# Performance work log

Measured on AMD Instinct MI355X. Metric: run time of the kernel, lower is better.

## Reference

```python
import jax, jax.numpy as jnp
import numpy as np

N_USER = 27094
M_SPOT = 42852
N_EDGE = 2_000_000
D_FEAT = 128


def setup_inputs() -> dict:
    key = jax.random.key(0)
    k1, k2, k3, k4 = jax.random.split(key, 4)
    spot_x = jax.random.normal(k1, (M_SPOT, D_FEAT), dtype=jnp.float32)
    user_x = jax.random.normal(k2, (N_USER, D_FEAT), dtype=jnp.float32)
    u_idx = jax.random.randint(k3, (N_EDGE,), 0, N_USER, dtype=jnp.int32)
    s_idx = jax.random.randint(k4, (N_EDGE,), 0, M_SPOT, dtype=jnp.int32)
    user_spot = jnp.stack([u_idx, s_idx], axis=0)  # [2, E]
    return {"spot_x": spot_x, "user_x": user_x, "user_spot": user_spot}


def reference(spot_x, user_x, user_spot):
    u = user_spot[0]  # [E] user index per edge
    s = user_spot[1]  # [E] spot index per edge
    # symmetric GCN normalization: 1/sqrt(deg_u * deg_s) per edge
    user_deg = jnp.bincount(u, length=N_USER)
    spot_deg = jnp.bincount(s, length=M_SPOT)
    div = jnp.sqrt((user_deg[u] * spot_deg[s]).astype(spot_x.dtype))[:, None]  # [E,1]
    # spot -> user aggregation
    source_spot = spot_x[s] / div                                   # [E, D]
    user_out = jax.ops.segment_sum(source_spot, u, num_segments=N_USER)
    # user -> spot aggregation
    source_user = user_x[u] / div                                   # [E, D]
    spot_out = jax.ops.segment_sum(source_user, s, num_segments=M_SPOT)
    return (spot_out, user_out)
```

## Files before the change

### kernel.cpp

```cpp
#include <hip/hip_runtime.h>
#include <stdint.h>


#define NPB_LOG2 6
#define NPB 64
#define MAXB 768
#define PART_CHUNK 2048
#define BH_CHUNK 16384
#define SORT_CAP 8192
#define SORT2_CAP 16384

__device__ __forceinline__ ushort f2bf(float f) {
    uint32_t u = __float_as_uint(f);
    return (ushort)((u + 0x7fffu + ((u >> 16) & 1u)) >> 16);
}

__global__ __launch_bounds__(256) void bhist_kernel(
        const int* __restrict__ u, const int* __restrict__ s, int E,
        int nbu, int nbs, int* __restrict__ bd) {
    __shared__ int hist[2 * MAXB];
    const int tid = threadIdx.x;
    const int nb = nbu + nbs;
    const int beg = blockIdx.x * BH_CHUNK;
    const int end = min(beg + BH_CHUNK, E);
    for (int b = tid; b < nb; b += 256) hist[b] = 0;
    __syncthreads();
    for (int i = beg + tid; i < end; i += 256) {
        atomicAdd(&hist[u[i] >> NPB_LOG2], 1);
        atomicAdd(&hist[nbu + (s[i] >> NPB_LOG2)], 1);
    }
    __syncthreads();
    for (int b = tid; b < nb; b += 256) {
        int h = hist[b];
        if (h) atomicAdd(&bd[b], h);
    }
}

__global__ __launch_bounds__(1024) void scan2_kernel(
        const int* __restrict__ bd, int nbu, int nbs,
        int* __restrict__ buoff, int* __restrict__ bsoff,
        int* __restrict__ gcu, int* __restrict__ gcs) {
    __shared__ int wsums[16];
    __shared__ int total;
    const int tid = threadIdx.x, lane = tid & 63, wid = tid >> 6;
    const int n   = blockIdx.x ? nbs : nbu;
    const int* in = blockIdx.x ? (bd + nbu) : bd;
    int* out = blockIdx.x ? bsoff : buoff;
    int* gc  = blockIdx.x ? gcs   : gcu;
    int v = (tid < n) ? in[tid] : 0;
    int x = v;
#pragma unroll
    for (int d = 1; d < 64; d <<= 1) {
        int t = __shfl_up(x, d);
        if (lane >= d) x += t;
    }
    if (lane == 63) wsums[wid] = x;
    __syncthreads();
    if (tid == 0) {
        int run = 0;
#pragma unroll
        for (int w = 0; w < 16; ++w) { int t = wsums[w]; wsums[w] = run; run += t; }
        total = run;
    }
    __syncthreads();
    int excl = wsums[wid] + (x - v);
    if (tid < n) { out[tid] = excl; gc[tid] = excl; }
    if (tid == 0) out[n] = total;
}

__global__ void convert_kernel(const float* __restrict__ x, const float* __restrict__ isd,
                               ushort* __restrict__ xb, int n_rows) {
    int idx = blockIdx.x * blockDim.x + threadIdx.x;
    if (idx >= (n_rows << 6)) return;
    int row = idx >> 6, c = idx & 63;
    float w = isd[row];
    const float* xr = x + ((size_t)row << 7);
    ushort2 o;
    o.x = f2bf(xr[c] * w);
    o.y = f2bf(xr[c + 64] * w);
    *reinterpret_cast<ushort2*>(xb + ((size_t)row << 7) + 2 * c) = o;
}

__global__ __launch_bounds__(256) void part_kernel(
        const int* __restrict__ prim, const int* __restrict__ sec, int E,
        int nb, int* __restrict__ gcur, uint32_t* __restrict__ out) {
    __shared__ int hist[MAXB];
    __shared__ int loff[MAXB];
    __shared__ int gbase[MAXB];
    __shared__ int cur[MAXB];
    __shared__ int wsum[4];
    __shared__ uint32_t sbuf[PART_CHUNK];
    const int tid = threadIdx.x;
    const int lane = tid & 63;
    const int wid = tid >> 6;
    const int beg = blockIdx.x * PART_CHUNK;
    const int end = min(beg + PART_CHUNK, E);
    const int cnt_total = end - beg;
    for (int b = tid; b < nb; b += 256) hist[b] = 0;
    __syncthreads();
    for (int i = beg + tid; i < end; i += 256)
        atomicAdd(&hist[prim[i] >> NPB_LOG2], 1);
    __syncthreads();
    {
        int b0 = tid * 3;
        int h0 = (b0 + 0 < nb) ? hist[b0 + 0] : 0;
        int h1 = (b0 + 1 < nb) ? hist[b0 + 1] : 0;
        int h2 = (b0 + 2 < nb) ? hist[b0 + 2] : 0;
        int tsum = h0 + h1 + h2;
        int x = tsum;
#pragma unroll
        for (int d = 1; d < 64; d <<= 1) {
            int t = __shfl_up(x, d);
            if (lane >= d) x += t;
        }
        if (lane == 63) wsum[wid] = x;
        __syncthreads();
        if (tid == 0) {
            int run = 0;
#pragma unroll
            for (int w = 0; w < 4; ++w) { int t = wsum[w]; wsum[w] = run; run += t; }
        }
        __syncthreads();
        int base = wsum[wid] + (x - tsum);
        if (b0 + 0 < nb) loff[b0 + 0] = base;
        if (b0 + 1 < nb) loff[b0 + 1] = base + h0;
        if (b0 + 2 < nb) loff[b0 + 2] = base + h0 + h1;
    }
    __syncthreads();
    for (int b = tid; b < nb; b += 256) {
        cur[b] = loff[b];
        int c = hist[b];
        gbase[b] = c > 0 ? atomicAdd(&gcur[b], c) : 0;
    }
    __syncthreads();
    for (int i = beg + tid; i < end; i += 256) {
        int p = prim[i], s = sec[i];
        int b = p >> NPB_LOG2;
        int l = atomicAdd(&cur[b], 1);
        sbuf[l] = ((uint32_t)p << 16) | (uint32_t)s;
    }
    __syncthreads();
    for (int k = tid; k < cnt_total; k += 256) {
        uint32_t p = sbuf[k];
        int b = (int)(p >> (16 + NPB_LOG2));
        out[gbase[b] + (k - loff[b])] = p;
    }
}

__global__ __launch_bounds__(256) void bdeg2_kernel(
        const uint32_t* __restrict__ bufU, const uint32_t* __restrict__ bufS,
        const int* __restrict__ buoff, const int* __restrict__ bsoff, int nbu,
        float* __restrict__ isd_u, float* __restrict__ isd_s, int N, int M) {
    __shared__ int hist[NPB];
    const int tid = threadIdx.x;
    const int b = blockIdx.x;
    const uint32_t* buf; const int* boff; float* isd; int n_rows; int bb;
    if (b < nbu) { buf = bufU; boff = buoff; isd = isd_u; n_rows = N; bb = b; }
    else         { buf = bufS; boff = bsoff; isd = isd_s; n_rows = M; bb = b - nbu; }
    const int jbeg = boff[bb];
    const int cnt = boff[bb + 1] - jbeg;
    if (tid < NPB) hist[tid] = 0;
    __syncthreads();
    for (int k = tid; k < cnt; k += 256)
        atomicAdd(&hist[(buf[jbeg + k] >> 16) & (NPB - 1)], 1);
    __syncthreads();
    if (tid < NPB) {
        int node = (bb << NPB_LOG2) + tid;
        if (node < n_rows) {
            int h = hist[tid];
            isd[node] = h > 0 ? rsqrtf((float)h) : 0.f;
        }
    }
}

__global__ __launch_bounds__(512) void fscan2_kernel(
        const ushort* __restrict__ xbs, const ushort* __restrict__ xbu,
        const uint32_t* __restrict__ bufU, const uint32_t* __restrict__ bufS,
        const int* __restrict__ buoff, const int* __restrict__ bsoff, int nbu,
        float* __restrict__ user_out, float* __restrict__ spot_out) {
    __shared__ ushort srt[SORT2_CAP];
    __shared__ int hist[NPB];
    __shared__ int scur[NPB];
    __shared__ float isdl[NPB];
    const int tid = threadIdx.x;
    const int b = blockIdx.x;
    const ushort* xb; const uint32_t* buf; const int* boff; float* out; int bb;
    if (b < nbu) { xb = xbs; buf = bufU; boff = buoff; out = user_out; bb = b; }
    else         { xb = xbu; buf = bufS; boff = bsoff; out = spot_out; bb = b - nbu; }
    const int jbeg = boff[bb];
    const int cnt = boff[bb + 1] - jbeg;
    if (cnt <= 0) return;
    const bool fits = (cnt <= SORT2_CAP);
    if (tid < NPB) hist[tid] = 0;
    __syncthreads();
    for (int k = tid; k < cnt; k += 512)
        atomicAdd(&hist[(buf[jbeg + k] >> 16) & (NPB - 1)], 1);
    __syncthreads();
    if (tid < NPB) {
        int h = hist[tid];
        int x = h;
#pragma unroll
        for (int d = 1; d < 64; d <<= 1) {
            int t = __shfl_up(x, d);
            if (tid >= d) x += t;
        }
        scur[tid] = x - h;
        isdl[tid] = h > 0 ? rsqrtf((float)h) : 0.f;
    }
    __syncthreads();
    if (fits) {
        for (int k = tid; k < cnt; k += 512) {
            uint32_t p = buf[jbeg + k];
            int slot = atomicAdd(&scur[(p >> 16) & (NPB - 1)], 1);
            srt[slot] = (ushort)p;
        }
    }
    __syncthreads();
    const int wid = tid >> 6, lane = tid & 63;
    const int rowbase = bb << NPB_LOG2;

#define ROWX(sv) (*reinterpret_cast<const uint32_t*>( \
        xb + (((size_t)(sv)) << 7) + (lane << 1)))
#define UPX(rv) __uint_as_float((rv) << 16)
#define UPY(rv) __uint_as_float((rv) & 0xffff0000u)

    if (fits) {
        for (int ld = wid; ld < NPB; ld += 8) {
            const int deg = hist[ld];
            if (!deg) continue;
            const int off0 = scur[ld] - deg;
            const float w = isdl[ld];
            float ax = 0.f, ay = 0.f;
            int j = 0;
            if (deg >= 16) {
                ushort c0 = srt[off0+0], c1 = srt[off0+1], c2 = srt[off0+2], c3 = srt[off0+3],
                       c4 = srt[off0+4], c5 = srt[off0+5], c6 = srt[off0+6], c7 = srt[off0+7];
                uint32_t r0 = ROWX(c0), r1 = ROWX(c1), r2 = ROWX(c2), r3 = ROWX(c3),
                         r4 = ROWX(c4), r5 = ROWX(c5), r6 = ROWX(c6), r7 = ROWX(c7);
                for (j = 8; j + 8 <= deg; j += 8) {
                    const int q = off0 + j;
                    ushort n0 = srt[q+0], n1 = srt[q+1], n2 = srt[q+2], n3 = srt[q+3],
                           n4 = srt[q+4], n5 = srt[q+5], n6 = srt[q+6], n7 = srt[q+7];
                    uint32_t s0 = ROWX(n0), s1 = ROWX(n1), s2 = ROWX(n2), s3 = ROWX(n3),
                             s4 = ROWX(n4), s5 = ROWX(n5), s6 = ROWX(n6), s7 = ROWX(n7);
                    ax += ((UPX(r0) + UPX(r1)) + (UPX(r2) + UPX(r3)))
                        + ((UPX(r4) + UPX(r5)) + (UPX(r6) + UPX(r7)));
                    ay += ((UPY(r0) + UPY(r1)) + (UPY(r2) + UPY(r3)))
                        + ((UPY(r4) + UPY(r5)) + (UPY(r6) + UPY(r7)));
                    r0 = s0; r1 = s1; r2 = s2; r3 = s3;
                    r4 = s4; r5 = s5; r6 = s6; r7 = s7;
                }
                ax += ((UPX(r0) + UPX(r1)) + (UPX(r2) + UPX(r3)))
                    + ((UPX(r4) + UPX(r5)) + (UPX(r6) + UPX(r7)));
                ay += ((UPY(r0) + UPY(r1)) + (UPY(r2) + UPY(r3)))
                    + ((UPY(r4) + UPY(r5)) + (UPY(r6) + UPY(r7)));
            }
            for (; j < deg; ++j) {
                uint32_t r = ROWX(srt[off0 + j]);
                ax += UPX(r); ay += UPY(r);
            }
            const size_t ro = ((size_t)(rowbase + ld)) << 7;
            out[ro + lane]      = ax * w;
            out[ro + 64 + lane] = ay * w;
        }
    } else {
        const int cs = (cnt + 7) >> 3;
        const int beg = wid * cs;
        const int end = min(beg + cs, cnt);
        if (beg >= end) return;
        float ax = 0.f, ay = 0.f;
        int curd = (int)(buf[jbeg + beg] >> 16);
        for (int k = beg; k < end; ++k) {
            uint32_t p = buf[jbeg + k];
            int d_ = (int)(p >> 16);
            if (d_ != curd) {
                float w_ = isdl[curd & (NPB - 1)];
                unsafeAtomicAdd(out + ((size_t)curd << 7) + lane, ax * w_);
                unsafeAtomicAdd(out + ((size_t)curd << 7) + 64 + lane, ay * w_);
                ax = 0.f; ay = 0.f; curd = d_;
            }
            uint32_t r = ROWX((ushort)p);
            ax += UPX(r); ay += UPY(r);
        }
        float w_ = isdl[curd & (NPB - 1)];
        unsafeAtomicAdd(out + ((size_t)curd << 7) + lane, ax * w_);
        unsafeAtomicAdd(out + ((size_t)curd << 7) + 64 + lane, ay * w_);
    }
#undef UPY
#undef UPX
#undef ROWX
}


__global__ __launch_bounds__(256) void bdeg_kernel(
        const uint32_t* __restrict__ buf, const int* __restrict__ boff,
        float* __restrict__ isd, int n_rows) {
    __shared__ int hist[NPB];
    const int tid = threadIdx.x;
    const int jbeg = boff[blockIdx.x];
    const int cnt = boff[blockIdx.x + 1] - jbeg;
    if (tid < NPB) hist[tid] = 0;
    __syncthreads();
    for (int k = tid; k < cnt; k += 256)
        atomicAdd(&hist[(buf[jbeg + k] >> 16) & (NPB - 1)], 1);
    __syncthreads();
    if (tid < NPB) {
        int node = (blockIdx.x << NPB_LOG2) + tid;
        if (node < n_rows) {
            int h = hist[tid];
            isd[node] = h > 0 ? rsqrtf((float)h) : 0.f;
        }
    }
}

__global__ __launch_bounds__(512) void fscan_kernel(
        const ushort* __restrict__ xb, const uint32_t* __restrict__ buf,
        const int* __restrict__ boff, float* __restrict__ isd_out,
        float* __restrict__ out, int n_rows) {
    __shared__ uint32_t sorted[SORT_CAP];
    __shared__ int hist[NPB];
    __shared__ int scur[NPB];
    __shared__ float isdl[NPB];
    const int tid = threadIdx.x;
    const int jbeg = boff[blockIdx.x];
    const int cnt = boff[blockIdx.x + 1] - jbeg;
    if (cnt <= 0) {
        if (tid < NPB) {
            int node = (blockIdx.x << NPB_LOG2) + tid;
            if (node < n_rows) isd_out[node] = 0.f;
        }
        return;
    }
    const bool fits = (cnt <= SORT_CAP);
    if (tid < NPB) hist[tid] = 0;
    __syncthreads();
    for (int k = tid; k < cnt; k += 512)
        atomicAdd(&hist[(buf[jbeg + k] >> 16) & (NPB - 1)], 1);
    __syncthreads();
    if (tid < NPB) {
        int h = hist[tid];
        int x = h;
#pragma unroll
        for (int d = 1; d < 64; d <<= 1) {
            int t = __shfl_up(x, d);
            if (tid >= d) x += t;
        }
        scur[tid] = x - h;
        float iv = h > 0 ? rsqrtf((float)h) : 0.f;
        isdl[tid] = iv;
        int node = (blockIdx.x << NPB_LOG2) + tid;
        if (node < n_rows) isd_out[node] = iv;
    }
    __syncthreads();
    if (fits) {
        for (int k = tid; k < cnt; k += 512) {
            uint32_t p = buf[jbeg + k];
            int slot = atomicAdd(&scur[(p >> 16) & (NPB - 1)], 1);
            sorted[slot] = p;
        }
    }
    __syncthreads();
    const int wid = tid >> 6, lane = tid & 63;
    const int cs = (cnt + 7) >> 3;
    const int beg = wid * cs;
    const int end = min(beg + cs, cnt);
    if (beg >= end) return;

#define QLD(i) (fits ? sorted[i] : buf[jbeg + (i)])
#define ROW(pv) (*reinterpret_cast<const uint32_t*>( \
        xb + (((size_t)((pv) & 0xffffu)) << 7) + (lane << 1)))
#define UPX(rv) __uint_as_float((rv) << 16)
#define UPY(rv) __uint_as_float((rv) & 0xffff0000u)
    float ax = 0.f, ay = 0.f;
    int curd = (int)(QLD(beg) >> 16);
    for (int k = beg; k < end; ++k) {
        uint32_t p = QLD(k);
        int d_ = (int)(p >> 16);
        if (d_ != curd) {
            float w_ = isdl[curd & (NPB - 1)];
            unsafeAtomicAdd(out + ((size_t)curd << 7) + lane, ax * w_);
            unsafeAtomicAdd(out + ((size_t)curd << 7) + 64 + lane, ay * w_);
            ax = 0.f; ay = 0.f; curd = d_;
        }
        uint32_t r = ROW(p);
        ax += UPX(r); ay += UPY(r);
    }
    float w_ = isdl[curd & (NPB - 1)];
    unsafeAtomicAdd(out + ((size_t)curd << 7) + lane, ax * w_);
    unsafeAtomicAdd(out + ((size_t)curd << 7) + 64 + lane, ay * w_);
#undef UPY
#undef UPX
#undef ROW
#undef QLD
}


__global__ void deg_kernel(const int* __restrict__ u, const int* __restrict__ s,
                           int E, int* __restrict__ udeg, int* __restrict__ sdeg) {
    int i = blockIdx.x * blockDim.x + threadIdx.x;
    if (i < E) {
        atomicAdd(&udeg[u[i]], 1);
        atomicAdd(&sdeg[s[i]], 1);
    }
}

__global__ void init_isd_kernel(const int* __restrict__ udeg, const int* __restrict__ sdeg,
                                float* __restrict__ isd_u, float* __restrict__ isd_s,
                                int n_user, int m_spot) {
    int i = blockIdx.x * blockDim.x + threadIdx.x;
    if (i < n_user) { int d = udeg[i]; isd_u[i] = d > 0 ? rsqrtf((float)d) : 0.f; }
    if (i < m_spot) { int d = sdeg[i]; isd_s[i] = d > 0 ? rsqrtf((float)d) : 0.f; }
}

__global__ __launch_bounds__(256) void scatter_kernel(const float* __restrict__ spot_x,
                                                      const float* __restrict__ user_x,
                                                      const int* __restrict__ u,
                                                      const int* __restrict__ s, int E,
                                                      const float* __restrict__ isd_u,
                                                      const float* __restrict__ isd_s,
                                                      float* __restrict__ spot_out,
                                                      float* __restrict__ user_out) {
    const int lane = threadIdx.x & 63;
    const int e = blockIdx.x * 4 + (threadIdx.x >> 6);
    if (e >= E) return;
    const int uu = u[e], ss = s[e];
    const float w = isd_u[uu] * isd_s[ss];
    const float2 sv = *reinterpret_cast<const float2*>(spot_x + (size_t)ss * 128 + lane * 2);
    const float2 uv = *reinterpret_cast<const float2*>(user_x + (size_t)uu * 128 + lane * 2);
    atomicAdd(&user_out[(size_t)uu * 128 + lane * 2 + 0], sv.x * w);
    atomicAdd(&user_out[(size_t)uu * 128 + lane * 2 + 1], sv.y * w);
    atomicAdd(&spot_out[(size_t)ss * 128 + lane * 2 + 0], uv.x * w);
    atomicAdd(&spot_out[(size_t)ss * 128 + lane * 2 + 1], uv.y * w);
}

static inline char* align256(char* p) {
    return (char*)(((uintptr_t)p + 255u) & ~(uintptr_t)255u);
}

extern "C" void kernel_launch(void* const* d_in, const int* in_sizes, int n_in,
                              void* d_out, int out_size, void* d_ws, size_t ws_size,
                              hipStream_t stream) {
    const float* spot_x = (const float*)d_in[0];
    const float* user_x = (const float*)d_in[1];
    const int*   edges  = (const int*)d_in[2];
    const int M = in_sizes[0] / 128;
    const int N = in_sizes[1] / 128;
    const int E = in_sizes[2] / 2;
    const int* u = edges;
    const int* s = edges + E;
    float* spot_out = (float*)d_out;
    float* user_out = (float*)d_out + (size_t)M * 128;

    const int nbu = (N + NPB - 1) / NPB;
    const int nbs = (M + NPB - 1) / NPB;
    const int nm = (N > M) ? N : M;
    const int gpart = (E + PART_CHUNK - 1) / PART_CHUNK;

    char* ws = (char*)d_ws;
    float*    isd_u = (float*)ws; ws = align256(ws + sizeof(float) * (size_t)N);
    float*    isd_s = (float*)ws; ws = align256(ws + sizeof(float) * (size_t)M);
    int*      bd    = (int*)ws;   ws = align256(ws + sizeof(int) * (size_t)(nbu + nbs));
    int*      buoff = (int*)ws;   ws = align256(ws + sizeof(int) * (size_t)(nbu + 1));
    int*      bsoff = (int*)ws;   ws = align256(ws + sizeof(int) * (size_t)(nbs + 1));
    int*      gcu   = (int*)ws;   ws = align256(ws + sizeof(int) * (size_t)nbu);
    int*      gcs   = (int*)ws;   ws = align256(ws + sizeof(int) * (size_t)nbs);
    uint32_t* bufU  = (uint32_t*)ws; ws = align256(ws + sizeof(uint32_t) * (size_t)E);
    uint32_t* bufS  = (uint32_t*)ws; ws = align256(ws + sizeof(uint32_t) * (size_t)E);
    ushort*   xbs   = (ushort*)ws;
    ushort*   xbu   = (ushort*)align256((char*)xbs + sizeof(ushort) * ((size_t)M * 128));
    size_t tierA_needed = (size_t)((char*)xbu - (char*)d_ws)
                        + sizeof(ushort) * ((size_t)N * 128);
    size_t tierB_needed = (size_t)((char*)xbs - (char*)d_ws)
                        + sizeof(ushort) * ((size_t)nm * 128);

    if (tierB_needed <= ws_size && nbu <= MAXB && nbs <= MAXB) {
        hipMemsetAsync(bd, 0, sizeof(int) * (size_t)(nbu + nbs), stream);
        hipMemsetAsync(d_out, 0, sizeof(float) * (size_t)out_size, stream);
        bhist_kernel<<<(E + BH_CHUNK - 1) / BH_CHUNK, 256, 0, stream>>>(
            u, s, E, nbu, nbs, bd);
        scan2_kernel<<<2, 1024, 0, stream>>>(bd, nbu, nbs, buoff, bsoff, gcu, gcs);
        part_kernel<<<gpart, 256, 0, stream>>>(u, s, E, nbu, gcu, bufU);
        part_kernel<<<gpart, 256, 0, stream>>>(s, u, E, nbs, gcs, bufS);
        if (tierA_needed <= ws_size) {
            bdeg2_kernel<<<nbu + nbs, 256, 0, stream>>>(
                bufU, bufS, buoff, bsoff, nbu, isd_u, isd_s, N, M);
            convert_kernel<<<((M << 6) + 255) / 256, 256, 0, stream>>>(spot_x, isd_s, xbs, M);
            convert_kernel<<<((N << 6) + 255) / 256, 256, 0, stream>>>(user_x, isd_u, xbu, N);
            fscan2_kernel<<<nbu + nbs, 512, 0, stream>>>(
                xbs, xbu, bufU, bufS, buoff, bsoff, nbu, user_out, spot_out);
        } else {
            ushort* xb = xbs;
            bdeg_kernel<<<nbs, 256, 0, stream>>>(bufS, bsoff, isd_s, M);
            convert_kernel<<<((M << 6) + 255) / 256, 256, 0, stream>>>(spot_x, isd_s, xb, M);
            fscan_kernel<<<nbu, 512, 0, stream>>>(xb, bufU, buoff, isd_u, user_out, N);
            convert_kernel<<<((N << 6) + 255) / 256, 256, 0, stream>>>(user_x, isd_u, xb, N);
            fscan_kernel<<<nbs, 512, 0, stream>>>(xb, bufS, bsoff, isd_s, spot_out, M);
        }
        return;
    }

    {
        char* w2 = (char*)d_ws;
        int*   udeg2  = (int*)w2;   w2 += sizeof(int) * (size_t)N;
        int*   sdeg2  = (int*)w2;   w2 += sizeof(int) * (size_t)M;
        float* isd_u2 = (float*)w2; w2 += sizeof(float) * (size_t)N;
        float* isd_s2 = (float*)w2; w2 += sizeof(float) * (size_t)M;
        if ((size_t)(w2 - (char*)d_ws) <= ws_size) {
            hipMemsetAsync(udeg2, 0, sizeof(int) * (size_t)(N + M), stream);
            deg_kernel<<<(E + 255) / 256, 256, 0, stream>>>(u, s, E, udeg2, sdeg2);
            init_isd_kernel<<<(nm + 255) / 256, 256, 0, stream>>>(
                udeg2, sdeg2, isd_u2, isd_s2, N, M);
            hipMemsetAsync(d_out, 0, sizeof(float) * (size_t)out_size, stream);
            scatter_kernel<<<((size_t)E + 3) / 4, 256, 0, stream>>>(
                spot_x, user_x, u, s, E, isd_u2, isd_s2, spot_out, user_out);
        }
    }
}
```

Before: 282.0 us.

## Split gather buckets across multiple blocks, merge partition and convert kernels

The per-bucket gather kernel is replaced by one that splits each 64-node bucket across several blocks (about 2048 blocks per direction). Each block register-sorts its slice and accumulates into the output with atomic adds instead of plain stores. The two partition launches are fused into one kernel that reads u and s once, and the two convert launches are merged into one. The goals are more parallelism and occupancy in the gather phase and fewer launches and index reads. In exchange, the gather now issues more global float atomics on rows shared between sub-blocks and uses more shared memory in the partition kernel.

```diff
diff --git a/kernel.cpp b/kernel.cpp
--- a/kernel.cpp
+++ b/kernel.cpp
@@ -8,7 +8,7 @@
 #define PART_CHUNK 2048
 #define BH_CHUNK 16384
 #define SORT_CAP 8192
-#define SORT2_CAP 16384
+#define RCAP 4096
 
 __device__ __forceinline__ ushort f2bf(float f) {
     uint32_t u = __float_as_uint(f);
@@ -68,6 +68,24 @@
     if (tid == 0) out[n] = total;
 }
 
+__global__ void convert2_kernel(const float* __restrict__ spot_x,
+                                const float* __restrict__ user_x,
+                                const float* __restrict__ isd_s,
+                                const float* __restrict__ isd_u,
+                                ushort* __restrict__ xbs, ushort* __restrict__ xbu,
+                                int M, int N) {
+    int idx = blockIdx.x * blockDim.x + threadIdx.x;
+    if (idx >= ((M + N) << 6)) return;
+    int row = idx >> 6, c = idx & 63;
+    const float* x; float w; ushort* xb;
+    if (row < M) { x = spot_x + ((size_t)row << 7); w = isd_s[row]; xb = xbs + ((size_t)row << 7); }
+    else { row -= M; x = user_x + ((size_t)row << 7); w = isd_u[row]; xb = xbu + ((size_t)row << 7); }
+    ushort2 o;
+    o.x = f2bf(x[c] * w);
+    o.y = f2bf(x[c + 64] * w);
+    *reinterpret_cast<ushort2*>(xb + 2 * c) = o;
+}
+
 __global__ void convert_kernel(const float* __restrict__ x, const float* __restrict__ isd,
                                ushort* __restrict__ xb, int n_rows) {
     int idx = blockIdx.x * blockDim.x + threadIdx.x;
@@ -81,27 +99,33 @@
     *reinterpret_cast<ushort2*>(xb + ((size_t)row << 7) + 2 * c) = o;
 }
 
-__global__ __launch_bounds__(256) void part_kernel(
-        const int* __restrict__ prim, const int* __restrict__ sec, int E,
-        int nb, int* __restrict__ gcur, uint32_t* __restrict__ out) {
-    __shared__ int hist[MAXB];
-    __shared__ int loff[MAXB];
-    __shared__ int gbase[MAXB];
-    __shared__ int cur[MAXB];
+__global__ __launch_bounds__(256) void part2_kernel(
+        const int* __restrict__ u, const int* __restrict__ s, int E,
+        int nbu, int nbs, int* __restrict__ gcu, int* __restrict__ gcs,
+        uint32_t* __restrict__ outU, uint32_t* __restrict__ outS) {
+    __shared__ int histU[MAXB], loffU[MAXB], gbaseU[MAXB], curU[MAXB];
+    __shared__ int histS[MAXB], loffS[MAXB], gbaseS[MAXB], curS[MAXB];
     __shared__ int wsum[4];
-    __shared__ uint32_t sbuf[PART_CHUNK];
+    __shared__ uint32_t sbufU[PART_CHUNK];
+    __shared__ uint32_t sbufS[PART_CHUNK];
     const int tid = threadIdx.x;
     const int lane = tid & 63;
     const int wid = tid >> 6;
     const int beg = blockIdx.x * PART_CHUNK;
     const int end = min(beg + PART_CHUNK, E);
     const int cnt_total = end - beg;
-    for (int b = tid; b < nb; b += 256) hist[b] = 0;
-    __syncthreads();
-    for (int i = beg + tid; i < end; i += 256)
-        atomicAdd(&hist[prim[i] >> NPB_LOG2], 1);
-    __syncthreads();
-    {
+    for (int b = tid; b < nbu; b += 256) histU[b] = 0;
+    for (int b = tid; b < nbs; b += 256) histS[b] = 0;
+    __syncthreads();
+    for (int i = beg + tid; i < end; i += 256) {
+        atomicAdd(&histU[u[i] >> NPB_LOG2], 1);
+        atomicAdd(&histS[s[i] >> NPB_LOG2], 1);
+    }
+    __syncthreads();
+    for (int dir = 0; dir < 2; ++dir) {
+        int nb = dir ? nbs : nbu;
+        int* hist = dir ? histS : histU;
+        int* loff = dir ? loffS : loffU;
         int b0 = tid * 3;
         int h0 = (b0 + 0 < nb) ? hist[b0 + 0] : 0;
         int h1 = (b0 + 1 < nb) ? hist[b0 + 1] : 0;
@@ -125,25 +149,34 @@
         if (b0 + 0 < nb) loff[b0 + 0] = base;
         if (b0 + 1 < nb) loff[b0 + 1] = base + h0;
         if (b0 + 2 < nb) loff[b0 + 2] = base + h0 + h1;
-    }
-    __syncthreads();
-    for (int b = tid; b < nb; b += 256) {
-        cur[b] = loff[b];
-        int c = hist[b];
-        gbase[b] = c > 0 ? atomicAdd(&gcur[b], c) : 0;
+        __syncthreads();
+    }
+    for (int b = tid; b < nbu; b += 256) {
+        curU[b] = loffU[b];
+        int c = histU[b];
+        gbaseU[b] = c > 0 ? atomicAdd(&gcu[b], c) : 0;
+    }
+    for (int b = tid; b < nbs; b += 256) {
+        curS[b] = loffS[b];
+        int c = histS[b];
+        gbaseS[b] = c > 0 ? atomicAdd(&gcs[b], c) : 0;
     }
     __syncthreads();
     for (int i = beg + tid; i < end; i += 256) {
-        int p = prim[i], s = sec[i];
-        int b = p >> NPB_LOG2;
-        int l = atomicAdd(&cur[b], 1);
-        sbuf[l] = ((uint32_t)p << 16) | (uint32_t)s;
+        int uu = u[i], ss = s[i];
+        int lu = atomicAdd(&curU[uu >> NPB_LOG2], 1);
+        sbufU[lu] = ((uint32_t)uu << 16) | (uint32_t)ss;
+        int ls = atomicAdd(&curS[ss >> NPB_LOG2], 1);
+        sbufS[ls] = ((uint32_t)ss << 16) | (uint32_t)uu;
     }
     __syncthreads();
     for (int k = tid; k < cnt_total; k += 256) {
-        uint32_t p = sbuf[k];
+        uint32_t p = sbufU[k];
         int b = (int)(p >> (16 + NPB_LOG2));
-        out[gbase[b] + (k - loff[b])] = p;
+        outU[gbaseU[b] + (k - loffU[b])] = p;
+        uint32_t q = sbufS[k];
+        int b2 = (int)(q >> (16 + NPB_LOG2));
+        outS[gbaseS[b2] + (k - loffS[b2])] = q;
     }
 }
 
@@ -173,63 +206,69 @@
     }
 }
 
-__global__ __launch_bounds__(512) void fscan2_kernel(
-        const ushort* __restrict__ xbs, const ushort* __restrict__ xbu,
-        const uint32_t* __restrict__ bufU, const uint32_t* __restrict__ bufS,
-        const int* __restrict__ buoff, const int* __restrict__ bsoff, int nbu,
-        float* __restrict__ user_out, float* __restrict__ spot_out) {
-    __shared__ ushort srt[SORT2_CAP];
+__global__ __launch_bounds__(512) void fscan3_kernel(
+        const ushort* __restrict__ xb, const uint32_t* __restrict__ buf,
+        const int* __restrict__ boff, const float* __restrict__ isd,
+        float* __restrict__ out, int split) {
+    __shared__ ushort srt[RCAP];
     __shared__ int hist[NPB];
     __shared__ int scur[NPB];
-    __shared__ float isdl[NPB];
     const int tid = threadIdx.x;
-    const int b = blockIdx.x;
-    const ushort* xb; const uint32_t* buf; const int* boff; float* out; int bb;
-    if (b < nbu) { xb = xbs; buf = bufU; boff = buoff; out = user_out; bb = b; }
-    else         { xb = xbu; buf = bufS; boff = bsoff; out = spot_out; bb = b - nbu; }
-    const int jbeg = boff[bb];
-    const int cnt = boff[bb + 1] - jbeg;
+    const int bucket = blockIdx.x / split;
+    const int sub = blockIdx.x - bucket * split;
+    const int jb = boff[bucket];
+    const int cnt = boff[bucket + 1] - jb;
     if (cnt <= 0) return;
-    const bool fits = (cnt <= SORT2_CAP);
-    if (tid < NPB) hist[tid] = 0;
-    __syncthreads();
-    for (int k = tid; k < cnt; k += 512)
-        atomicAdd(&hist[(buf[jbeg + k] >> 16) & (NPB - 1)], 1);
-    __syncthreads();
-    if (tid < NPB) {
-        int h = hist[tid];
-        int x = h;
-#pragma unroll
-        for (int d = 1; d < 64; d <<= 1) {
-            int t = __shfl_up(x, d);
-            if (tid >= d) x += t;
-        }
-        scur[tid] = x - h;
-        isdl[tid] = h > 0 ? rsqrtf((float)h) : 0.f;
-    }
-    __syncthreads();
-    if (fits) {
-        for (int k = tid; k < cnt; k += 512) {
-            uint32_t p = buf[jbeg + k];
-            int slot = atomicAdd(&scur[(p >> 16) & (NPB - 1)], 1);
-            srt[slot] = (ushort)p;
-        }
-    }
-    __syncthreads();
+    const int sbeg = jb + (int)((long long)cnt * sub / split);
+    const int send = jb + (int)((long long)cnt * (sub + 1) / split);
+    const int scnt = send - sbeg;
+    if (scnt <= 0) return;
     const int wid = tid >> 6, lane = tid & 63;
-    const int rowbase = bb << NPB_LOG2;
+    const int rowbase = bucket << NPB_LOG2;
 
 #define ROWX(sv) (*reinterpret_cast<const uint32_t*>( \
         xb + (((size_t)(sv)) << 7) + (lane << 1)))
 #define UPX(rv) __uint_as_float((rv) << 16)
 #define UPY(rv) __uint_as_float((rv) & 0xffff0000u)
 
-    if (fits) {
+    if (scnt <= RCAP) {
+        if (tid < NPB) hist[tid] = 0;
+        __syncthreads();
+        uint32_t ereg[8];
+#pragma unroll
+        for (int k = 0; k < 8; ++k) {
+            int idx = sbeg + (k << 9) + tid;
+            if (idx < send) {
+                ereg[k] = buf[idx];
+                atomicAdd(&hist[(ereg[k] >> 16) & (NPB - 1)], 1);
+            } else ereg[k] = 0u;
+        }
+        __syncthreads();
+        if (tid < NPB) {
+            int h = hist[tid];
+            int x = h;
+#pragma unroll
+            for (int d = 1; d < 64; d <<= 1) {
+                int t = __shfl_up(x, d);
+                if (tid >= d) x += t;
+            }
+            scur[tid] = x - h;
+        }
+        __syncthreads();
+#pragma unroll
+        for (int k = 0; k < 8; ++k) {
+            int idx = sbeg + (k << 9) + tid;
+            if (idx < send) {
+                uint32_t p = ereg[k];
+                int slot = atomicAdd(&scur[(p >> 16) & (NPB - 1)], 1);
+                srt[slot] = (ushort)p;
+            }
+        }
+        __syncthreads();
         for (int ld = wid; ld < NPB; ld += 8) {
             const int deg = hist[ld];
             if (!deg) continue;
             const int off0 = scur[ld] - deg;
-            const float w = isdl[ld];
             float ax = 0.f, ay = 0.f;
             int j = 0;
             if (deg >= 16) {
@@ -259,22 +298,23 @@
                 uint32_t r = ROWX(srt[off0 + j]);
                 ax += UPX(r); ay += UPY(r);
             }
+            const float w = isd[rowbase + ld];
             const size_t ro = ((size_t)(rowbase + ld)) << 7;
-            out[ro + lane]      = ax * w;
-            out[ro + 64 + lane] = ay * w;
+            unsafeAtomicAdd(out + ro + lane,      ax * w);
+            unsafeAtomicAdd(out + ro + 64 + lane, ay * w);
         }
     } else {
-        const int cs = (cnt + 7) >> 3;
-        const int beg = wid * cs;
-        const int end = min(beg + cs, cnt);
+        const int cs = (scnt + 7) >> 3;
+        const int beg = sbeg + wid * cs;
+        const int end = min(beg + cs, send);
         if (beg >= end) return;
         float ax = 0.f, ay = 0.f;
-        int curd = (int)(buf[jbeg + beg] >> 16);
+        int curd = (int)(buf[beg] >> 16);
         for (int k = beg; k < end; ++k) {
-            uint32_t p = buf[jbeg + k];
+            uint32_t p = buf[k];
             int d_ = (int)(p >> 16);
             if (d_ != curd) {
-                float w_ = isdl[curd & (NPB - 1)];
+                float w_ = isd[curd];
                 unsafeAtomicAdd(out + ((size_t)curd << 7) + lane, ax * w_);
                 unsafeAtomicAdd(out + ((size_t)curd << 7) + 64 + lane, ay * w_);
                 ax = 0.f; ay = 0.f; curd = d_;
@@ -282,7 +322,7 @@
             uint32_t r = ROWX((ushort)p);
             ax += UPX(r); ay += UPY(r);
         }
-        float w_ = isdl[curd & (NPB - 1)];
+        float w_ = isd[curd];
         unsafeAtomicAdd(out + ((size_t)curd << 7) + lane, ax * w_);
         unsafeAtomicAdd(out + ((size_t)curd << 7) + 64 + lane, ay * w_);
     }
@@ -479,15 +519,18 @@
         bhist_kernel<<<(E + BH_CHUNK - 1) / BH_CHUNK, 256, 0, stream>>>(
             u, s, E, nbu, nbs, bd);
         scan2_kernel<<<2, 1024, 0, stream>>>(bd, nbu, nbs, buoff, bsoff, gcu, gcs);
-        part_kernel<<<gpart, 256, 0, stream>>>(u, s, E, nbu, gcu, bufU);
-        part_kernel<<<gpart, 256, 0, stream>>>(s, u, E, nbs, gcs, bufS);
+        part2_kernel<<<gpart, 256, 0, stream>>>(u, s, E, nbu, nbs, gcu, gcs, bufU, bufS);
         if (tierA_needed <= ws_size) {
             bdeg2_kernel<<<nbu + nbs, 256, 0, stream>>>(
                 bufU, bufS, buoff, bsoff, nbu, isd_u, isd_s, N, M);
-            convert_kernel<<<((M << 6) + 255) / 256, 256, 0, stream>>>(spot_x, isd_s, xbs, M);
-            convert_kernel<<<((N << 6) + 255) / 256, 256, 0, stream>>>(user_x, isd_u, xbu, N);
-            fscan2_kernel<<<nbu + nbs, 512, 0, stream>>>(
-                xbs, xbu, bufU, bufS, buoff, bsoff, nbu, user_out, spot_out);
+            convert2_kernel<<<(((M + N) << 6) + 255) / 256, 256, 0, stream>>>(
+                spot_x, user_x, isd_s, isd_u, xbs, xbu, M, N);
+            int splitU = 2048 / nbu; if (splitU < 1) splitU = 1; if (splitU > 16) splitU = 16;
+            int splitS = 2048 / nbs; if (splitS < 1) splitS = 1; if (splitS > 16) splitS = 16;
+            fscan3_kernel<<<nbu * splitU, 512, 0, stream>>>(
+                xbs, bufU, buoff, isd_u, user_out, splitU);
+            fscan3_kernel<<<nbs * splitS, 512, 0, stream>>>(
+                xbu, bufS, bsoff, isd_s, spot_out, splitS);
         } else {
             ushort* xb = xbs;
             bdeg_kernel<<<nbs, 256, 0, stream>>>(bufS, bsoff, isd_s, M);
```

Measured after the change: 293.6 us. 4.1% more time.
